# Kernel optimization log

Measured on AMD Instinct MI355X. Metric: run time of the kernel, lower is better.

## Reference

```python
import jax, jax.numpy as jnp
import numpy as np

N_NODES = 50000
N_EDGES = 800000  # undirected edge count E0
D_FEAT = 64
K_STEPS = 10
LAMBDA = 3.0


def setup_inputs() -> dict:
    key = jax.random.key(0)
    k1, k2, k3 = jax.random.split(key, 3)
    x = jax.random.normal(k1, (N_NODES, D_FEAT), dtype=jnp.float32)
    edge_src = jax.random.randint(k2, (N_EDGES,), 0, N_NODES)
    edge_dst = jax.random.randint(k3, (N_EDGES,), 0, N_NODES)
    return {"x": x, "edge_src": edge_src, "edge_dst": edge_dst}


def _forward(x, edge_src, edge_dst):
    N, D = x.shape
    # --- symmetric adjacency (directed edge list, both orientations) ---
    row = jnp.concatenate([edge_src, edge_dst])
    col = jnp.concatenate([edge_dst, edge_src])
    # degree with self loops (fill_diag/add_self_loops weight 1), shared by
    # gcn_norm and inc_norm in the original code
    deg = jax.ops.segment_sum(jnp.ones(row.shape[0], x.dtype), row, num_segments=N) + 1.0
    dis = deg ** -0.5  # deg_inv_sqrt, [N]
    # gcn-normalized adjacency weights D^-1/2 (A+I) D^-1/2
    w = dis[row] * dis[col]          # off-diagonal edge weights [2*E0]
    w_self = dis * dis               # self-loop weights [N]

    def adj_mv(v):  # edge_index @ v
        return jax.ops.segment_sum(w[:, None] * v[col], row, num_segments=N) + w_self[:, None] * v

    # --- normalized incidence matrix (one row per undirected edge) ---
    r = jnp.maximum(edge_src, edge_dst)  # row_index after row>=col mask
    c = jnp.minimum(edge_src, edge_dst)
    a = dis[r]  # +1 entry scaled by deg_inv_sqrt of column r
    b = dis[c]  # -1 entry scaled by deg_inv_sqrt of column c

    def inc_mv(v):  # inc_mat @ v -> [E0, D]
        return a[:, None] * v[r] - b[:, None] * v[c]

    def incT_mv(z):  # inc_mat.t() @ z -> [N, D]
        return (jax.ops.segment_sum(a[:, None] * z, r, num_segments=N)
                - jax.ops.segment_sum(b[:, None] * z, c, num_segments=N))

    def l21_projection(z):
        rn = jnp.linalg.norm(z, axis=1)                 # row L2 norms [E0]
        s = jnp.minimum(rn, LAMBDA)
        s = jnp.where(rn > 0, s / jnp.where(rn > 0, rn, 1.0), s)
        return s[:, None] * z

    hh = x
    z0 = jnp.zeros((edge_src.shape[0], D), x.dtype)

    def step(carry, _):
        xk, zk = carry
        y = 0.25 * hh + 0.75 * adj_mv(xk)
        x_bar = y - 0.25 * incT_mv(zk)
        z_bar = zk + 2.0 * inc_mv(x_bar)
        zk = l21_projection(z_bar)
        xk = y - 0.25 * incT_mv(zk)
        return (xk, zk), None

    (xK, _), _ = jax.lax.scan(step, (x, z0), None, length=K_STEPS)
    return xK


def reference(x, edge_src, edge_dst):
    return _forward(x, edge_src, edge_dst)
```

## Files before the change

### kernel.cpp

```cpp
#include <hip/hip_runtime.h>
#include <hip/hip_fp16.h>
#include <math.h>

constexpr int NN = 50000;
constexpr int NE = 800000;
constexpr int KS = 10;
constexpr float LAM = 3.0f;

constexpr int SCAN_NB = (NN + 255) / 256;
constexpr int NODE_NB = NN * 64 / 256;


__global__ __launch_bounds__(256) void countRC_kernel(
    const int* __restrict__ src, const int* __restrict__ dst,
    int* __restrict__ cR, int* __restrict__ cC) {
  int e = blockIdx.x * 256 + threadIdx.x;
  if (e >= NE) return;
  int s = src[e], d = dst[e];
  int r = s > d ? s : d;
  int c = s > d ? d : s;
  atomicAdd(&cR[r], 1);
  atomicAdd(&cC[c], 1);
}

__global__ __launch_bounds__(256) void dis_kernel(
    const int* __restrict__ cR, const int* __restrict__ cC,
    float* __restrict__ dis) {
  int i = blockIdx.x * 256 + threadIdx.x;
  if (i < NN) dis[i] = 1.0f / sqrtf((float)(cR[i] + cC[i] + 1));
}

__global__ __launch_bounds__(256) void half_copy_kernel(
    const float* __restrict__ X, __half* __restrict__ XHlo,
    __half* __restrict__ XHhi) {
  int i = blockIdx.x * 256 + threadIdx.x;
  if (i >= NN * 16) return;
  float4 v = ((const float4*)X)[i];
  __half2 h0 = __floats2half2_rn(v.x, v.y);
  __half2 h1 = __floats2half2_rn(v.z, v.w);
  uint2 o;
  o.x = *(const unsigned*)&h0;
  o.y = *(const unsigned*)&h1;
  int w = i >> 4, f4 = i & 15;
  __half* dst = (f4 < 8) ? XHlo : XHhi;
  ((uint2*)dst)[w * 8 + (f4 & 7)] = o;
}


__global__ __launch_bounds__(256) void scanA_kernel(
    const int* __restrict__ cnt, int* __restrict__ bsum) {
  __shared__ int sm[256];
  int t = threadIdx.x;
  int i = blockIdx.x * 256 + t;
  int v = (i < NN) ? cnt[i] : 0;
  sm[t] = v;
  __syncthreads();
  for (int off = 128; off > 0; off >>= 1) {
    if (t < off) sm[t] += sm[t + off];
    __syncthreads();
  }
  if (t == 0) bsum[blockIdx.x] = sm[0];
}

__global__ __launch_bounds__(256) void scanB_kernel(
    int* __restrict__ bsum, int* __restrict__ boff) {
  __shared__ int sm[256];
  int t = threadIdx.x;
  int v = (t < SCAN_NB) ? bsum[t] : 0;
  sm[t] = v;
  __syncthreads();
  for (int off = 1; off < 256; off <<= 1) {
    int a = (t >= off) ? sm[t - off] : 0;
    __syncthreads();
    sm[t] += a;
    __syncthreads();
  }
  if (t < SCAN_NB) boff[t] = sm[t] - v;
}

__global__ __launch_bounds__(256) void scanC_kernel(
    const int* __restrict__ cnt, const int* __restrict__ boff,
    int* __restrict__ ptr, int* __restrict__ cur) {
  __shared__ int sm[256];
  int t = threadIdx.x;
  int i = blockIdx.x * 256 + t;
  int v = (i < NN) ? cnt[i] : 0;
  sm[t] = v;
  __syncthreads();
  for (int off = 1; off < 256; off <<= 1) {
    int a = (t >= off) ? sm[t - off] : 0;
    __syncthreads();
    sm[t] += a;
    __syncthreads();
  }
  if (i < NN) {
    int ex = boff[blockIdx.x] + sm[t] - v;
    ptr[i] = ex;
    cur[i] = ex;
    if (i == NN - 1) ptr[NN] = ex + v;
  }
}

__global__ __launch_bounds__(256) void sortscatter_kernel(
    const int* __restrict__ src, const int* __restrict__ dst,
    const float* __restrict__ dis,
    int* __restrict__ urR, int* __restrict__ uC,
    int2* __restrict__ cb8, int2* __restrict__ cEnt) {
  int e = blockIdx.x * 256 + threadIdx.x;
  if (e >= NE) return;
  int s = src[e], d = dst[e];
  int r = s > d ? s : d;
  int c = s > d ? d : s;
  int p = atomicAdd(&urR[r], 1);
  cb8[p] = make_int2(c, __float_as_int(dis[c]));
  int q = atomicAdd(&uC[c], 1);
  cEnt[q] = make_int2(r, p);
}


template <int FIRST>
__global__ __launch_bounds__(256) void adj_kernel(
    const __half* __restrict__ XHlo, const __half* __restrict__ XHhi,
    const float* __restrict__ H, const float* __restrict__ U,
    const float* __restrict__ dis,
    const int* __restrict__ rPtr, const int* __restrict__ cPtr,
    const int2* __restrict__ cEnt, const int2* __restrict__ cb8,
    float* __restrict__ XB, __half* __restrict__ XBh) {
  int bid = blockIdx.x;
  int half = (bid >= NODE_NB) ? 1 : 0;
  int w = (int)(((unsigned)(bid - half * NODE_NB) * 256u + threadIdx.x) >> 6);
  if (w >= NN) return;
  int lane = threadIdx.x & 63;
  int g = lane >> 3, l = lane & 7;
  const uint2* XH2 = (const uint2*)(half ? XHhi : XHlo);
  int rb = rPtr[w], lenR = rPtr[w + 1] - rb;
  int cb = cPtr[w], lenC = cPtr[w + 1] - cb;
  int total = lenR + lenC;
  int lr1 = lenR > 0 ? lenR - 1 : 0;
  int lc1 = lenC > 0 ? lenC - 1 : 0;
  float ax = 0.f, ay = 0.f, az = 0.f, aw = 0.f;

#define ADJ_FETCH(T, NB, WT)                                         \
  {                                                                  \
    int tr = (T) < lr1 ? (T) : lr1;                                  \
    int tc = (T) - lenR; tc = tc > 0 ? tc : 0; tc = tc < lc1 ? tc : lc1; \
    int2 rcv = cb8[rb + tr];                                         \
    int2 ce = cEnt[cb + tc];                                         \
    bool isR = (T) < lenR;                                           \
    NB = isR ? rcv.x : ce.x;                                         \
    WT = isR ? __int_as_float(rcv.y) : dis[ce.x];                    \
  }
#define ADJ_ACC(XV, W)                                               \
  {                                                                  \
    float2 p = __half22float2(*(const __half2*)&XV.x);               \
    float2 q = __half22float2(*(const __half2*)&XV.y);               \
    ax = fmaf(W, p.x, ax); ay = fmaf(W, p.y, ay);                    \
    az = fmaf(W, q.x, az); aw = fmaf(W, q.y, aw);                    \
  }

  int t = g;
  for (; t + 8 < total; t += 16) {
    int n0, n1; float w0, w1;
    ADJ_FETCH(t, n0, w0);
    ADJ_FETCH(t + 8, n1, w1);
    uint2 x0 = XH2[n0 * 8 + l];
    uint2 x1 = XH2[n1 * 8 + l];
    ADJ_ACC(x0, w0);
    ADJ_ACC(x1, w1);
  }
  for (; t < total; t += 8) {
    int n0; float w0;
    ADJ_FETCH(t, n0, w0);
    uint2 x0 = XH2[n0 * 8 + l];
    ADJ_ACC(x0, w0);
  }
#undef ADJ_FETCH
#undef ADJ_ACC

  ax += __shfl_xor(ax, 8, 64); ay += __shfl_xor(ay, 8, 64);
  az += __shfl_xor(az, 8, 64); aw += __shfl_xor(aw, 8, 64);
  ax += __shfl_xor(ax, 16, 64); ay += __shfl_xor(ay, 16, 64);
  az += __shfl_xor(az, 16, 64); aw += __shfl_xor(aw, 16, 64);
  ax += __shfl_xor(ax, 32, 64); ay += __shfl_xor(ay, 32, 64);
  az += __shfl_xor(az, 32, 64); aw += __shfl_xor(aw, 32, 64);
  if (g == 0) {
    float di = dis[w];
    int idx = w * 16 + half * 8 + l;
    uint2 xsu = XH2[w * 8 + l];
    float2 xsa = __half22float2(*(const __half2*)&xsu.x);
    float2 xsb = __half22float2(*(const __half2*)&xsu.y);
    float4 h4 = ((const float4*)H)[idx];
    float4 y4;
    y4.x = 0.25f * h4.x + 0.75f * di * fmaf(di, xsa.x, ax);
    y4.y = 0.25f * h4.y + 0.75f * di * fmaf(di, xsa.y, ay);
    y4.z = 0.25f * h4.z + 0.75f * di * fmaf(di, xsb.x, az);
    y4.w = 0.25f * h4.w + 0.75f * di * fmaf(di, xsb.y, aw);
    float4 xb;
    if (FIRST) {
      xb = y4;
    } else {
      float4 u4 = ((const float4*)U)[idx];
      xb.x = y4.x - 0.25f * u4.x;
      xb.y = y4.y - 0.25f * u4.y;
      xb.z = y4.z - 0.25f * u4.z;
      xb.w = y4.w - 0.25f * u4.w;
    }
    ((float4*)XB)[idx] = xb;
    __half2 hb0 = __floats2half2_rn(xb.x, xb.y);
    __half2 hb1 = __floats2half2_rn(xb.z, xb.w);
    uint2 ob;
    ob.x = *(const unsigned*)&hb0;
    ob.y = *(const unsigned*)&hb1;
    ((uint2*)XBh)[idx] = ob;
  }
}

template <int FIRST>
__global__ __launch_bounds__(256) void zupd_kernel(
    __half* __restrict__ Z, const __half* __restrict__ XBh,
    const float* __restrict__ dis,
    const int* __restrict__ rPtr, const int2* __restrict__ cb8,
    float* __restrict__ U1) {
  int w = (int)((blockIdx.x * 256u + threadIdx.x) >> 6);
  if (w >= NN) return;
  int lane = threadIdx.x & 63;
  int g = lane >> 4, l = lane & 15;
  const uint2* X2 = (const uint2*)XBh;
  uint2* Z2 = (uint2*)Z;
  int rb = rPtr[w], re = rPtr[w + 1];
  float a = dis[w];
  uint2 xwu = X2[w * 16 + l];
  float2 xwa = __half22float2(*(const __half2*)&xwu.x);
  float2 xwb = __half22float2(*(const __half2*)&xwu.y);
  float sx = 0.f, sy = 0.f, sz = 0.f, sw = 0.f;
  for (int e = rb + g; e < re; e += 4) {
    int2 cbv = cb8[e];
    int c = cbv.x;
    float b = __int_as_float(cbv.y);
    uint2 xcu = X2[c * 16 + l];
    float2 xca = __half22float2(*(const __half2*)&xcu.x);
    float2 xcb = __half22float2(*(const __half2*)&xcu.y);
    float zx, zy, zz, zw;
    if (FIRST) {
      zx = zy = zz = zw = 0.f;
    } else {
      uint2 zu = Z2[e * 16 + l];
      float2 f0 = __half22float2(*(const __half2*)&zu.x);
      float2 f1 = __half22float2(*(const __half2*)&zu.y);
      zx = f0.x; zy = f0.y; zz = f1.x; zw = f1.y;
    }
    zx += 2.0f * (a * xwa.x - b * xca.x);
    zy += 2.0f * (a * xwa.y - b * xca.y);
    zz += 2.0f * (a * xwb.x - b * xcb.x);
    zw += 2.0f * (a * xwb.y - b * xcb.y);
    float ss = zx * zx + zy * zy + zz * zz + zw * zw;
    ss += __shfl_xor(ss, 1, 64);
    ss += __shfl_xor(ss, 2, 64);
    ss += __shfl_xor(ss, 4, 64);
    ss += __shfl_xor(ss, 8, 64);
    float rn = sqrtf(ss);
    float sc = (rn > LAM) ? (LAM / rn) : 1.0f;
    zx *= sc; zy *= sc; zz *= sc; zw *= sc;
    __half2 o0 = __floats2half2_rn(zx, zy);
    __half2 o1 = __floats2half2_rn(zz, zw);
    uint2 outu;
    outu.x = *(const unsigned*)&o0;
    outu.y = *(const unsigned*)&o1;
    Z2[e * 16 + l] = outu;
    sx += zx; sy += zy; sz += zz; sw += zw;
  }
  sx += __shfl_xor(sx, 16, 64); sy += __shfl_xor(sy, 16, 64);
  sz += __shfl_xor(sz, 16, 64); sw += __shfl_xor(sw, 16, 64);
  sx += __shfl_xor(sx, 32, 64); sy += __shfl_xor(sy, 32, 64);
  sz += __shfl_xor(sz, 32, 64); sw += __shfl_xor(sw, 32, 64);
  if (g == 0) {
    ((float4*)U1)[w * 16 + l] = make_float4(sx, sy, sz, sw);
  }
}

template <int FIRST, int LAST>
__global__ __launch_bounds__(256) void cside_kernel(
    const __half* __restrict__ Z, const float* __restrict__ XB,
    const float* __restrict__ dis,
    const int* __restrict__ cPtr, const int2* __restrict__ cEnt,
    const float* __restrict__ U1, float* __restrict__ U,
    float* __restrict__ Xout, __half* __restrict__ XHlo,
    __half* __restrict__ XHhi) {
  int w = (int)((blockIdx.x * 256u + threadIdx.x) >> 6);
  if (w >= NN) return;
  int lane = threadIdx.x & 63;
  int g = lane >> 4, l = lane & 15;
  const uint2* Z2 = (const uint2*)Z;
  int cb = cPtr[w], ce = cPtr[w + 1];
  float sx = 0.f, sy = 0.f, sz = 0.f, sw = 0.f;
  int j = cb + g;
  for (; j + 12 < ce; j += 16) {
    int e0 = cEnt[j].y;
    int e1 = cEnt[j + 4].y;
    int e2 = cEnt[j + 8].y;
    int e3 = cEnt[j + 12].y;
    uint2 zu0 = Z2[e0 * 16 + l];
    uint2 zu1 = Z2[e1 * 16 + l];
    uint2 zu2 = Z2[e2 * 16 + l];
    uint2 zu3 = Z2[e3 * 16 + l];
    float2 a0 = __half22float2(*(const __half2*)&zu0.x);
    float2 b0 = __half22float2(*(const __half2*)&zu0.y);
    float2 a1 = __half22float2(*(const __half2*)&zu1.x);
    float2 b1 = __half22float2(*(const __half2*)&zu1.y);
    float2 a2 = __half22float2(*(const __half2*)&zu2.x);
    float2 b2 = __half22float2(*(const __half2*)&zu2.y);
    float2 a3 = __half22float2(*(const __half2*)&zu3.x);
    float2 b3 = __half22float2(*(const __half2*)&zu3.y);
    sx += a0.x + a1.x + a2.x + a3.x;
    sy += a0.y + a1.y + a2.y + a3.y;
    sz += b0.x + b1.x + b2.x + b3.x;
    sw += b0.y + b1.y + b2.y + b3.y;
  }
  for (; j < ce; j += 4) {
    int e0 = cEnt[j].y;
    uint2 zu0 = Z2[e0 * 16 + l];
    float2 a0 = __half22float2(*(const __half2*)&zu0.x);
    float2 b0 = __half22float2(*(const __half2*)&zu0.y);
    sx += a0.x; sy += a0.y; sz += b0.x; sw += b0.y;
  }
  sx += __shfl_xor(sx, 16, 64); sy += __shfl_xor(sy, 16, 64);
  sz += __shfl_xor(sz, 16, 64); sw += __shfl_xor(sw, 16, 64);
  sx += __shfl_xor(sx, 32, 64); sy += __shfl_xor(sy, 32, 64);
  sz += __shfl_xor(sz, 32, 64); sw += __shfl_xor(sw, 32, 64);
  if (g == 0) {
    float di = dis[w];
    int idx = w * 16 + l;
    float4 u1 = ((const float4*)U1)[idx];
    float4 u;
    u.x = di * (u1.x - sx);
    u.y = di * (u1.y - sy);
    u.z = di * (u1.z - sz);
    u.w = di * (u1.w - sw);
    float4 xb = ((const float4*)XB)[idx];
    float4 y4;
    if (FIRST) {
      y4 = xb;
    } else {
      float4 uo = ((const float4*)U)[idx];
      y4.x = xb.x + 0.25f * uo.x;
      y4.y = xb.y + 0.25f * uo.y;
      y4.z = xb.z + 0.25f * uo.z;
      y4.w = xb.w + 0.25f * uo.w;
    }
    float4 o;
    o.x = y4.x - 0.25f * u.x;
    o.y = y4.y - 0.25f * u.y;
    o.z = y4.z - 0.25f * u.z;
    o.w = y4.w - 0.25f * u.w;
    if (LAST) {
      ((float4*)Xout)[idx] = o;
    } else {
      ((float4*)U)[idx] = u;
      __half2 h0 = __floats2half2_rn(o.x, o.y);
      __half2 h1 = __floats2half2_rn(o.z, o.w);
      uint2 oh;
      oh.x = *(const unsigned*)&h0;
      oh.y = *(const unsigned*)&h1;
      __half* dst = (l < 8) ? XHlo : XHhi;
      ((uint2*)dst)[w * 8 + (l & 7)] = oh;
    }
  }
}


extern "C" void kernel_launch(void* const* d_in, const int* in_sizes, int n_in,
                              void* d_out, int out_size, void* d_ws, size_t ws_size,
                              hipStream_t stream) {
  const float* x  = (const float*)d_in[0];
  const int* esrc = (const int*)d_in[1];
  const int* edst = (const int*)d_in[2];
  float* out = (float*)d_out;

  char* base = (char*)d_ws;
  size_t off = 0;
  auto carve = [&](size_t bytes) -> void* {
    void* p = base + off;
    off += (bytes + 255) & ~(size_t)255;
    return p;
  };
  __half* Z    = (__half*)carve((size_t)NE * 64 * 2);
  float* XB    = (float*)carve((size_t)NN * 64 * 4);
  float* U     = (float*)carve((size_t)NN * 64 * 4);
  float* U1    = (float*)carve((size_t)NN * 64 * 4);
  __half* XHlo = (__half*)carve((size_t)NN * 32 * 2);
  __half* XHhi = (__half*)carve((size_t)NN * 32 * 2);
  __half* XBh  = (__half*)carve((size_t)NN * 64 * 2);
  float* dis = (float*)carve((size_t)NN * 4);
  int* cR  = (int*)carve((size_t)NN * 4);
  int* cC  = (int*)carve((size_t)NN * 4);
  int* rPtr = (int*)carve((size_t)(NN + 1) * 4);
  int* cPtr = (int*)carve((size_t)(NN + 1) * 4);
  int* urR = (int*)carve((size_t)NN * 4);
  int* uC  = (int*)carve((size_t)NN * 4);
  int* bsum = (int*)carve((size_t)SCAN_NB * 4);
  int* boff = (int*)carve((size_t)SCAN_NB * 4);
  int2* cb8  = (int2*)carve((size_t)NE * 8);
  int2* cEnt = (int2*)carve((size_t)NE * 8);
  (void)ws_size; (void)in_sizes; (void)n_in; (void)out_size;

  hipMemsetAsync(cR, 0, NN * 4, stream);
  hipMemsetAsync(cC, 0, NN * 4, stream);

  const int edgeGrid = (NE + 255) / 256;
  countRC_kernel<<<edgeGrid, 256, 0, stream>>>(esrc, edst, cR, cC);
  dis_kernel<<<(NN + 255) / 256, 256, 0, stream>>>(cR, cC, dis);
  half_copy_kernel<<<(NN * 16 + 255) / 256, 256, 0, stream>>>(x, XHlo, XHhi);
  scanA_kernel<<<SCAN_NB, 256, 0, stream>>>(cR, bsum);
  scanB_kernel<<<1, 256, 0, stream>>>(bsum, boff);
  scanC_kernel<<<SCAN_NB, 256, 0, stream>>>(cR, boff, rPtr, urR);
  scanA_kernel<<<SCAN_NB, 256, 0, stream>>>(cC, bsum);
  scanB_kernel<<<1, 256, 0, stream>>>(bsum, boff);
  scanC_kernel<<<SCAN_NB, 256, 0, stream>>>(cC, boff, cPtr, uC);
  sortscatter_kernel<<<edgeGrid, 256, 0, stream>>>(esrc, edst, dis, urR, uC,
                                                   cb8, cEnt);

  for (int k = 0; k < KS; ++k) {
    if (k == 0)
      adj_kernel<1><<<2 * NODE_NB, 256, 0, stream>>>(XHlo, XHhi, x, U, dis,
                                                     rPtr, cPtr, cEnt, cb8,
                                                     XB, XBh);
    else
      adj_kernel<0><<<2 * NODE_NB, 256, 0, stream>>>(XHlo, XHhi, x, U, dis,
                                                     rPtr, cPtr, cEnt, cb8,
                                                     XB, XBh);

    if (k == 0)
      zupd_kernel<1><<<NODE_NB, 256, 0, stream>>>(Z, XBh, dis, rPtr, cb8, U1);
    else
      zupd_kernel<0><<<NODE_NB, 256, 0, stream>>>(Z, XBh, dis, rPtr, cb8, U1);

    if (k == 0)
      cside_kernel<1, 0><<<NODE_NB, 256, 0, stream>>>(Z, XB, dis, cPtr, cEnt,
                                                      U1, U, out, XHlo, XHhi);
    else if (k == KS - 1)
      cside_kernel<0, 1><<<NODE_NB, 256, 0, stream>>>(Z, XB, dis, cPtr, cEnt,
                                                      U1, U, out, XHlo, XHhi);
    else
      cside_kernel<0, 0><<<NODE_NB, 256, 0, stream>>>(Z, XB, dis, cPtr, cEnt,
                                                      U1, U, out, XHlo, XHhi);
  }
}
```

Measured before the change: 1.548 ms.

## Merge half-split feature buffer, unroll gathers, interleave node order for balance

The fp16 copy of x was stored as two half-width buffers and processed by twice as many waves; it is now one contiguous 64-wide buffer gathered by one wave per node using 16 lanes per neighbour, with a 4-way unrolled gather loop. zupd is unrolled two edges deep with hoisted 2*dis scaling. zupd and cside map wave index to nodes alternating from both ends of the node range, which is meant to balance load given the max/min edge ordering. Fewer waves and merged rows reduce index reloads and duplicated neighbour-list traversal, at the cost of wider per-row gathers and more registers.

```diff
diff --git a/kernel.cpp b/kernel.cpp
--- a/kernel.cpp
+++ b/kernel.cpp
@@ -31,8 +31,7 @@
 }
 
 __global__ __launch_bounds__(256) void half_copy_kernel(
-    const float* __restrict__ X, __half* __restrict__ XHlo,
-    __half* __restrict__ XHhi) {
+    const float* __restrict__ X, __half* __restrict__ XH) {
   int i = blockIdx.x * 256 + threadIdx.x;
   if (i >= NN * 16) return;
   float4 v = ((const float4*)X)[i];
@@ -41,9 +40,7 @@
   uint2 o;
   o.x = *(const unsigned*)&h0;
   o.y = *(const unsigned*)&h1;
-  int w = i >> 4, f4 = i & 15;
-  __half* dst = (f4 < 8) ? XHlo : XHhi;
-  ((uint2*)dst)[w * 8 + (f4 & 7)] = o;
+  ((uint2*)XH)[i] = o;
 }
 
 
@@ -120,19 +117,16 @@
 
 template <int FIRST>
 __global__ __launch_bounds__(256) void adj_kernel(
-    const __half* __restrict__ XHlo, const __half* __restrict__ XHhi,
-    const float* __restrict__ H, const float* __restrict__ U,
-    const float* __restrict__ dis,
+    const __half* __restrict__ XH, const float* __restrict__ H,
+    const float* __restrict__ U, const float* __restrict__ dis,
     const int* __restrict__ rPtr, const int* __restrict__ cPtr,
     const int2* __restrict__ cEnt, const int2* __restrict__ cb8,
     float* __restrict__ XB, __half* __restrict__ XBh) {
-  int bid = blockIdx.x;
-  int half = (bid >= NODE_NB) ? 1 : 0;
-  int w = (int)(((unsigned)(bid - half * NODE_NB) * 256u + threadIdx.x) >> 6);
+  int w = (int)((blockIdx.x * 256u + threadIdx.x) >> 6);
   if (w >= NN) return;
   int lane = threadIdx.x & 63;
-  int g = lane >> 3, l = lane & 7;
-  const uint2* XH2 = (const uint2*)(half ? XHhi : XHlo);
+  int g = lane >> 4, l = lane & 15;
+  const uint2* XH2 = (const uint2*)XH;
   int rb = rPtr[w], lenR = rPtr[w + 1] - rb;
   int cb = cPtr[w], lenC = cPtr[w + 1] - cb;
   int total = lenR + lenC;
@@ -159,34 +153,38 @@
   }
 
   int t = g;
-  for (; t + 8 < total; t += 16) {
-    int n0, n1; float w0, w1;
+  for (; t + 12 < total; t += 16) {
+    int n0, n1, n2, n3; float w0, w1, w2, w3;
     ADJ_FETCH(t, n0, w0);
-    ADJ_FETCH(t + 8, n1, w1);
-    uint2 x0 = XH2[n0 * 8 + l];
-    uint2 x1 = XH2[n1 * 8 + l];
+    ADJ_FETCH(t + 4, n1, w1);
+    ADJ_FETCH(t + 8, n2, w2);
+    ADJ_FETCH(t + 12, n3, w3);
+    uint2 x0 = XH2[n0 * 16 + l];
+    uint2 x1 = XH2[n1 * 16 + l];
+    uint2 x2 = XH2[n2 * 16 + l];
+    uint2 x3 = XH2[n3 * 16 + l];
     ADJ_ACC(x0, w0);
     ADJ_ACC(x1, w1);
-  }
-  for (; t < total; t += 8) {
+    ADJ_ACC(x2, w2);
+    ADJ_ACC(x3, w3);
+  }
+  for (; t < total; t += 4) {
     int n0; float w0;
     ADJ_FETCH(t, n0, w0);
-    uint2 x0 = XH2[n0 * 8 + l];
+    uint2 x0 = XH2[n0 * 16 + l];
     ADJ_ACC(x0, w0);
   }
 #undef ADJ_FETCH
 #undef ADJ_ACC
 
-  ax += __shfl_xor(ax, 8, 64); ay += __shfl_xor(ay, 8, 64);
-  az += __shfl_xor(az, 8, 64); aw += __shfl_xor(aw, 8, 64);
   ax += __shfl_xor(ax, 16, 64); ay += __shfl_xor(ay, 16, 64);
   az += __shfl_xor(az, 16, 64); aw += __shfl_xor(aw, 16, 64);
   ax += __shfl_xor(ax, 32, 64); ay += __shfl_xor(ay, 32, 64);
   az += __shfl_xor(az, 32, 64); aw += __shfl_xor(aw, 32, 64);
   if (g == 0) {
     float di = dis[w];
-    int idx = w * 16 + half * 8 + l;
-    uint2 xsu = XH2[w * 8 + l];
+    int idx = w * 16 + l;
+    uint2 xsu = XH2[idx];
     float2 xsa = __half22float2(*(const __half2*)&xsu.x);
     float2 xsb = __half22float2(*(const __half2*)&xsu.y);
     float4 h4 = ((const float4*)H)[idx];
@@ -221,54 +219,79 @@
     const float* __restrict__ dis,
     const int* __restrict__ rPtr, const int2* __restrict__ cb8,
     float* __restrict__ U1) {
-  int w = (int)((blockIdx.x * 256u + threadIdx.x) >> 6);
-  if (w >= NN) return;
+  int i = (int)((blockIdx.x * 256u + threadIdx.x) >> 6);
+  if (i >= NN) return;
+  int w = (i & 1) ? (NN - 1 - (i >> 1)) : (i >> 1);
   int lane = threadIdx.x & 63;
   int g = lane >> 4, l = lane & 15;
   const uint2* X2 = (const uint2*)XBh;
   uint2* Z2 = (uint2*)Z;
   int rb = rPtr[w], re = rPtr[w + 1];
-  float a = dis[w];
+  float a2 = 2.0f * dis[w];
   uint2 xwu = X2[w * 16 + l];
   float2 xwa = __half22float2(*(const __half2*)&xwu.x);
   float2 xwb = __half22float2(*(const __half2*)&xwu.y);
+  float tx = a2 * xwa.x, ty = a2 * xwa.y;
+  float tz = a2 * xwb.x, tw = a2 * xwb.y;
   float sx = 0.f, sy = 0.f, sz = 0.f, sw = 0.f;
-  for (int e = rb + g; e < re; e += 4) {
-    int2 cbv = cb8[e];
-    int c = cbv.x;
-    float b = __int_as_float(cbv.y);
-    uint2 xcu = X2[c * 16 + l];
-    float2 xca = __half22float2(*(const __half2*)&xcu.x);
-    float2 xcb = __half22float2(*(const __half2*)&xcu.y);
-    float zx, zy, zz, zw;
-    if (FIRST) {
-      zx = zy = zz = zw = 0.f;
-    } else {
-      uint2 zu = Z2[e * 16 + l];
-      float2 f0 = __half22float2(*(const __half2*)&zu.x);
-      float2 f1 = __half22float2(*(const __half2*)&zu.y);
-      zx = f0.x; zy = f0.y; zz = f1.x; zw = f1.y;
+
+#define Z_PROC(E, CV, XCU, ZU)                                       \
+  {                                                                  \
+    float b2 = 2.0f * __int_as_float(CV.y);                          \
+    float2 xca = __half22float2(*(const __half2*)&XCU.x);            \
+    float2 xcb = __half22float2(*(const __half2*)&XCU.y);            \
+    float zx, zy, zz, zw;                                            \
+    if (FIRST) {                                                     \
+      zx = zy = zz = zw = 0.f;                                       \
+    } else {                                                         \
+      float2 f0 = __half22float2(*(const __half2*)&ZU.x);            \
+      float2 f1 = __half22float2(*(const __half2*)&ZU.y);            \
+      zx = f0.x; zy = f0.y; zz = f1.x; zw = f1.y;                    \
+    }                                                                \
+    zx += tx - b2 * xca.x;                                           \
+    zy += ty - b2 * xca.y;                                           \
+    zz += tz - b2 * xcb.x;                                           \
+    zw += tw - b2 * xcb.y;                                           \
+    float ss = zx * zx + zy * zy + zz * zz + zw * zw;                \
+    ss += __shfl_xor(ss, 1, 64);                                     \
+    ss += __shfl_xor(ss, 2, 64);                                     \
+    ss += __shfl_xor(ss, 4, 64);                                     \
+    ss += __shfl_xor(ss, 8, 64);                                     \
+    float rn = sqrtf(ss);                                            \
+    float sc = (rn > LAM) ? (LAM / rn) : 1.0f;                       \
+    zx *= sc; zy *= sc; zz *= sc; zw *= sc;                          \
+    __half2 o0 = __floats2half2_rn(zx, zy);                          \
+    __half2 o1 = __floats2half2_rn(zz, zw);                          \
+    uint2 outu;                                                      \
+    outu.x = *(const unsigned*)&o0;                                  \
+    outu.y = *(const unsigned*)&o1;                                  \
+    Z2[(E) * 16 + l] = outu;                                         \
+    sx += zx; sy += zy; sz += zz; sw += zw;                          \
+  }
+
+  int e = rb + g;
+  for (; e + 4 < re; e += 8) {
+    int2 cv0 = cb8[e];
+    int2 cv1 = cb8[e + 4];
+    uint2 xc0 = X2[cv0.x * 16 + l];
+    uint2 xc1 = X2[cv1.x * 16 + l];
+    uint2 zu0, zu1;
+    if (!FIRST) {
+      zu0 = Z2[e * 16 + l];
+      zu1 = Z2[(e + 4) * 16 + l];
     }
-    zx += 2.0f * (a * xwa.x - b * xca.x);
-    zy += 2.0f * (a * xwa.y - b * xca.y);
-    zz += 2.0f * (a * xwb.x - b * xcb.x);
-    zw += 2.0f * (a * xwb.y - b * xcb.y);
-    float ss = zx * zx + zy * zy + zz * zz + zw * zw;
-    ss += __shfl_xor(ss, 1, 64);
-    ss += __shfl_xor(ss, 2, 64);
-    ss += __shfl_xor(ss, 4, 64);
-    ss += __shfl_xor(ss, 8, 64);
-    float rn = sqrtf(ss);
-    float sc = (rn > LAM) ? (LAM / rn) : 1.0f;
-    zx *= sc; zy *= sc; zz *= sc; zw *= sc;
-    __half2 o0 = __floats2half2_rn(zx, zy);
-    __half2 o1 = __floats2half2_rn(zz, zw);
-    uint2 outu;
-    outu.x = *(const unsigned*)&o0;
-    outu.y = *(const unsigned*)&o1;
-    Z2[e * 16 + l] = outu;
-    sx += zx; sy += zy; sz += zz; sw += zw;
-  }
+    Z_PROC(e, cv0, xc0, zu0);
+    Z_PROC(e + 4, cv1, xc1, zu1);
+  }
+  if (e < re) {
+    int2 cv0 = cb8[e];
+    uint2 xc0 = X2[cv0.x * 16 + l];
+    uint2 zu0;
+    if (!FIRST) zu0 = Z2[e * 16 + l];
+    Z_PROC(e, cv0, xc0, zu0);
+  }
+#undef Z_PROC
+
   sx += __shfl_xor(sx, 16, 64); sy += __shfl_xor(sy, 16, 64);
   sz += __shfl_xor(sz, 16, 64); sw += __shfl_xor(sw, 16, 64);
   sx += __shfl_xor(sx, 32, 64); sy += __shfl_xor(sy, 32, 64);
@@ -284,10 +307,10 @@
     const float* __restrict__ dis,
     const int* __restrict__ cPtr, const int2* __restrict__ cEnt,
     const float* __restrict__ U1, float* __restrict__ U,
-    float* __restrict__ Xout, __half* __restrict__ XHlo,
-    __half* __restrict__ XHhi) {
-  int w = (int)((blockIdx.x * 256u + threadIdx.x) >> 6);
-  if (w >= NN) return;
+    float* __restrict__ Xout, __half* __restrict__ XH) {
+  int i = (int)((blockIdx.x * 256u + threadIdx.x) >> 6);
+  if (i >= NN) return;
+  int w = (i & 1) ? (NN - 1 - (i >> 1)) : (i >> 1);
   int lane = threadIdx.x & 63;
   int g = lane >> 4, l = lane & 15;
   const uint2* Z2 = (const uint2*)Z;
@@ -361,8 +384,7 @@
       uint2 oh;
       oh.x = *(const unsigned*)&h0;
       oh.y = *(const unsigned*)&h1;
-      __half* dst = (l < 8) ? XHlo : XHhi;
-      ((uint2*)dst)[w * 8 + (l & 7)] = oh;
+      ((uint2*)XH)[idx] = oh;
     }
   }
 }
@@ -383,13 +405,12 @@
     off += (bytes + 255) & ~(size_t)255;
     return p;
   };
-  __half* Z    = (__half*)carve((size_t)NE * 64 * 2);
-  float* XB    = (float*)carve((size_t)NN * 64 * 4);
-  float* U     = (float*)carve((size_t)NN * 64 * 4);
-  float* U1    = (float*)carve((size_t)NN * 64 * 4);
-  __half* XHlo = (__half*)carve((size_t)NN * 32 * 2);
-  __half* XHhi = (__half*)carve((size_t)NN * 32 * 2);
-  __half* XBh  = (__half*)carve((size_t)NN * 64 * 2);
+  __half* Z   = (__half*)carve((size_t)NE * 64 * 2);
+  float* XB   = (float*)carve((size_t)NN * 64 * 4);
+  float* U    = (float*)carve((size_t)NN * 64 * 4);
+  float* U1   = (float*)carve((size_t)NN * 64 * 4);
+  __half* XH  = (__half*)carve((size_t)NN * 64 * 2);
+  __half* XBh = (__half*)carve((size_t)NN * 64 * 2);
   float* dis = (float*)carve((size_t)NN * 4);
   int* cR  = (int*)carve((size_t)NN * 4);
   int* cC  = (int*)carve((size_t)NN * 4);
@@ -399,8 +420,8 @@
   int* uC  = (int*)carve((size_t)NN * 4);
   int* bsum = (int*)carve((size_t)SCAN_NB * 4);
   int* boff = (int*)carve((size_t)SCAN_NB * 4);
-  int2* cb8  = (int2*)carve((size_t)NE * 8);
-  int2* cEnt = (int2*)carve((size_t)NE * 8);
+  int2* cb8  = (int2*)carve((size_t)(NE + 4) * 8);
+  int2* cEnt = (int2*)carve((size_t)(NE + 4) * 8);
   (void)ws_size; (void)in_sizes; (void)n_in; (void)out_size;
 
   hipMemsetAsync(cR, 0, NN * 4, stream);
@@ -409,7 +430,7 @@
   const int edgeGrid = (NE + 255) / 256;
   countRC_kernel<<<edgeGrid, 256, 0, stream>>>(esrc, edst, cR, cC);
   dis_kernel<<<(NN + 255) / 256, 256, 0, stream>>>(cR, cC, dis);
-  half_copy_kernel<<<(NN * 16 + 255) / 256, 256, 0, stream>>>(x, XHlo, XHhi);
+  half_copy_kernel<<<(NN * 16 + 255) / 256, 256, 0, stream>>>(x, XH);
   scanA_kernel<<<SCAN_NB, 256, 0, stream>>>(cR, bsum);
   scanB_kernel<<<1, 256, 0, stream>>>(bsum, boff);
   scanC_kernel<<<SCAN_NB, 256, 0, stream>>>(cR, boff, rPtr, urR);
@@ -421,13 +442,11 @@
 
   for (int k = 0; k < KS; ++k) {
     if (k == 0)
-      adj_kernel<1><<<2 * NODE_NB, 256, 0, stream>>>(XHlo, XHhi, x, U, dis,
-                                                     rPtr, cPtr, cEnt, cb8,
-                                                     XB, XBh);
+      adj_kernel<1><<<NODE_NB, 256, 0, stream>>>(XH, x, U, dis, rPtr, cPtr,
+                                                 cEnt, cb8, XB, XBh);
     else
-      adj_kernel<0><<<2 * NODE_NB, 256, 0, stream>>>(XHlo, XHhi, x, U, dis,
-                                                     rPtr, cPtr, cEnt, cb8,
-                                                     XB, XBh);
+      adj_kernel<0><<<NODE_NB, 256, 0, stream>>>(XH, x, U, dis, rPtr, cPtr,
+                                                 cEnt, cb8, XB, XBh);
 
     if (k == 0)
       zupd_kernel<1><<<NODE_NB, 256, 0, stream>>>(Z, XBh, dis, rPtr, cb8, U1);
@@ -436,12 +455,12 @@
 
     if (k == 0)
       cside_kernel<1, 0><<<NODE_NB, 256, 0, stream>>>(Z, XB, dis, cPtr, cEnt,
-                                                      U1, U, out, XHlo, XHhi);
+                                                      U1, U, out, XH);
     else if (k == KS - 1)
       cside_kernel<0, 1><<<NODE_NB, 256, 0, stream>>>(Z, XB, dis, cPtr, cEnt,
-                                                      U1, U, out, XHlo, XHhi);
+                                                      U1, U, out, XH);
     else
       cside_kernel<0, 0><<<NODE_NB, 256, 0, stream>>>(Z, XB, dis, cPtr, cEnt,
-                                                      U1, U, out, XHlo, XHhi);
-  }
-}
+                                                      U1, U, out, XH);
+  }
+}
```

New measurement: 1.360 ms. -12.1%, faster.
